# Kernel optimization log

Hardware: AMD Instinct MI355X
Metric: run time of the kernel (lower is better)

## Reference

```python
import jax, jax.numpy as jnp
import numpy as np

NEG_INF = -1.0e12  # matches masked_fill value in the torch module


def _entmax15(x, axis=-1):
    """Exact entmax with alpha=1.5 (Peters & Martins, 2019), sort-based."""
    x = x - jnp.max(x, axis=axis, keepdims=True)
    x = x / 2.0
    d = x.shape[axis]
    xs = -jnp.sort(-x, axis=axis)  # descending sort along normalization axis
    rho = jnp.arange(1, d + 1, dtype=x.dtype)  # 1..d, broadcasts on last axis
    mean = jnp.cumsum(xs, axis=axis) / rho
    mean_sq = jnp.cumsum(xs * xs, axis=axis) / rho
    ss = rho * (mean_sq - mean * mean)
    delta = (1.0 - ss) / rho
    tau = mean - jnp.sqrt(jnp.clip(delta, 0.0))
    support = jnp.sum((tau <= xs).astype(jnp.int32), axis=axis, keepdims=True)
    tau_star = jnp.take_along_axis(tau, support - 1, axis=axis)
    y = jnp.clip(x - tau_star, 0.0)
    return y * y


def setup_inputs() -> dict:
    key = jax.random.key(0)
    kq, kk, kv, km = jax.random.split(key, 4)
    B, H, S, D = 4, 8, 1024, 128
    q = jax.random.normal(kq, (B, H, S, D), dtype=jnp.float32)
    k = jax.random.normal(kk, (B, H, S, D), dtype=jnp.float32)
    v = jax.random.normal(kv, (B, H, S, D), dtype=jnp.float32)
    mask = jax.random.randint(km, (B, 1, S, S), 0, 2, dtype=jnp.int32)
    return {"q": q, "k": k, "v": v, "mask": mask}


def reference(q, k, v, mask):
    D = q.shape[-1]
    scale = 1.0 / jnp.sqrt(jnp.asarray(D, dtype=q.dtype))
    scores = jnp.einsum("bhqd,bhkd->bhqk", q, k) * scale
    scores = jnp.where(mask == 0, jnp.asarray(NEG_INF, dtype=scores.dtype), scores)
    attn = _entmax15(scores, axis=-1)
    return jnp.einsum("bhqk,bhkd->bhqd", attn, v)
```

## Files before the change

### kernel.cpp

```cpp
#include <hip/hip_runtime.h>


#define S_ 1024
#define D_ 128
#define NEG_INF_F (-1.0e12f)
#define SCALE_F 0.08838834764831845f
#define NITER 14
#define CCAP 256

typedef float f32x4 __attribute__((ext_vector_type(4)));
typedef short short8 __attribute__((ext_vector_type(8)));

__device__ __forceinline__ ushort f2bf(float x) {
    unsigned u = __builtin_bit_cast(unsigned, x);
    u += 0x7FFFu + ((u >> 16) & 1u);
    return (ushort)(u >> 16);
}
__device__ __forceinline__ float bf2f(ushort h) {
    unsigned u = ((unsigned)h) << 16;
    return __builtin_bit_cast(float, u);
}

__global__ __launch_bounds__(256)
void pre_cvt(const float* __restrict__ K, const float* __restrict__ V,
             ushort* __restrict__ Kb, ushort* __restrict__ Vt)
{
    __shared__ __align__(16) ushort tileT[64][68];
    const int t = threadIdx.x;
    if (blockIdx.x < 4096) {
        int i = blockIdx.x * 256 + t;
        float4 v = ((const float4*)K)[i];
        ushort4 o;
        o.x = f2bf(v.x); o.y = f2bf(v.y); o.z = f2bf(v.z); o.w = f2bf(v.w);
        ((ushort4*)Kb)[i] = o;
        return;
    }
    const int vb = blockIdx.x - 4096;
    const int bh = vb >> 5, r5 = vb & 31, kt = r5 >> 1, dh = r5 & 1;
    const float* src = V + ((size_t)(bh * S_ + kt * 64)) * D_ + dh * 64;
    #pragma unroll
    for (int i = 0; i < 4; ++i) {
        int idx = t + i * 256, r = idx >> 4, c = idx & 15;
        float4 vv = *(const float4*)(src + (size_t)r * D_ + c * 4);
        tileT[c * 4 + 0][r] = f2bf(vv.x);
        tileT[c * 4 + 1][r] = f2bf(vv.y);
        tileT[c * 4 + 2][r] = f2bf(vv.z);
        tileT[c * 4 + 3][r] = f2bf(vv.w);
    }
    __syncthreads();
    ushort* dst = Vt + ((size_t)(bh * D_ + dh * 64)) * S_ + kt * 64;
    #pragma unroll
    for (int i = 0; i < 2; ++i) {
        int idx = t + i * 256, d = idx >> 3, jj = idx & 7;
        short8 val = *(const short8*)&tileT[d][jj * 8];
        *(short8*)(dst + (size_t)d * S_ + jj * 8) = val;
    }
}

__global__ __launch_bounds__(512, 6)
void entmax_attn(const float* __restrict__ Q, const ushort* __restrict__ Kb,
                 const ushort* __restrict__ Vt, const int* __restrict__ M,
                 float* __restrict__ O)
{
    __shared__ __align__(16) ushort sc[16][1024];
    __shared__ __align__(16) ushort kv[128][64];
    __shared__ __align__(16) ushort q_s[16][128];

    const int t = threadIdx.x;
    const int w = t >> 6, lane = t & 63, l = lane & 15, quad = lane >> 4;
    const int bh = blockIdx.x >> 6, qt = blockIdx.x & 63, b = bh >> 3;

    const ushort* kb_bh = Kb + (size_t)bh * S_ * D_;
    const ushort* vt_bh = Vt + (size_t)bh * D_ * S_;

    const int sr0 = t >> 3, sch = t & 7, sr1 = sr0 + 64;
    ushort* kvw0 = &kv[sr0][(sch ^ (sr0 & 7)) << 3];
    ushort* kvw1 = &kv[sr1][(sch ^ (sr0 & 7)) << 3];

    {
        const float4* qsrc = (const float4*)(Q + ((size_t)bh * S_ + (size_t)qt * 16) * D_);
        int r = t >> 5, c = t & 31;
        float4 v = qsrc[r * 32 + c];
        ushort4 o;
        o.x = f2bf(v.x); o.y = f2bf(v.y); o.z = f2bf(v.z); o.w = f2bf(v.w);
        *(ushort4*)&q_s[r][(((c >> 1) ^ (r & 7)) << 3) + ((c & 1) << 2)] = o;
    }
    short8 s0 = *(const short8*)(kb_bh + (size_t)sr0 * D_ + sch * 8);
    short8 s1 = *(const short8*)(kb_bh + (size_t)sr1 * D_ + sch * 8);
    *(short8*)kvw0 = s0;
    *(short8*)kvw1 = s1;
    __syncthreads();

    short8 aq[4];
    #pragma unroll
    for (int ks = 0; ks < 4; ++ks)
        aq[ks] = *(const short8*)&q_s[l][((ks * 4 + quad) ^ (l & 7)) << 3];

    const int n = w * 16 + l;
    const ushort* kvA = &kv[n][(quad ^ (l & 7)) << 3];
    const ushort* kvB = &kv[n][((4 + quad) ^ (l & 7)) << 3];

    #pragma unroll 1
    for (int kt = 0; kt < 8; ++kt) {
        f32x4 acc = {0.f, 0.f, 0.f, 0.f};
        #pragma unroll
        for (int kh = 0; kh < 2; ++kh) {
            const int h = kt * 2 + kh;
            if (h < 15) {
                const int h2 = h + 1;
                const ushort* nb = kb_bh + (size_t)(h2 >> 1) * (128 * D_) + (h2 & 1) * 64;
                s0 = *(const short8*)(nb + (size_t)sr0 * D_ + sch * 8);
                s1 = *(const short8*)(nb + (size_t)sr1 * D_ + sch * 8);
            }
            __builtin_amdgcn_s_setprio(1);
            {
                short8 bk0 = *(const short8*)kvA;
                short8 bk1 = *(const short8*)kvB;
                acc = __builtin_amdgcn_mfma_f32_16x16x32_bf16(aq[kh * 2 + 0], bk0, acc, 0, 0, 0);
                acc = __builtin_amdgcn_mfma_f32_16x16x32_bf16(aq[kh * 2 + 1], bk1, acc, 0, 0, 0);
            }
            __builtin_amdgcn_s_setprio(0);
            if (kh == 1) {
                #pragma unroll
                for (int r = 0; r < 4; ++r) {
                    const int rr = quad * 4 + r, col = kt * 128 + n;
                    sc[rr][(((col >> 3) ^ (rr & 7)) << 3) + (col & 7)] =
                        f2bf(acc[r] * SCALE_F);
                }
            }
            __syncthreads();
            if (h < 15) {
                *(short8*)kvw0 = s0;
                *(short8*)kvw1 = s1;
                __syncthreads();
            }
        }
    }

    s0 = *(const short8*)(vt_bh + (size_t)sr0 * S_ + sch * 8);
    s1 = *(const short8*)(vt_bh + (size_t)sr1 * S_ + sch * 8);

    const int row = t >> 5, u = t & 31;
    const int qg = qt * 16 + row;
    float x[32];
    #pragma unroll
    for (int c = 0; c < 4; ++c) {
        short8 v8 = *(const short8*)&sc[row][((c * 32 + u) ^ (row & 7)) << 3];
        #pragma unroll
        for (int e = 0; e < 8; ++e) x[c * 8 + e] = bf2f(((ushort*)&v8)[e]);
    }
    {
        const int4* mrow = (const int4*)(M + ((size_t)b * S_ + qg) * S_);
        #pragma unroll
        for (int c = 0; c < 4; ++c) {
            #pragma unroll
            for (int h = 0; h < 2; ++h) {
                int4 mm = mrow[c * 64 + u * 2 + h];
                if (mm.x == 0) x[c * 8 + h * 4 + 0] = NEG_INF_F;
                if (mm.y == 0) x[c * 8 + h * 4 + 1] = NEG_INF_F;
                if (mm.z == 0) x[c * 8 + h * 4 + 2] = NEG_INF_F;
                if (mm.w == 0) x[c * 8 + h * 4 + 3] = NEG_INF_F;
            }
        }
    }
    float mx = -3.0e38f;
    #pragma unroll
    for (int j = 0; j < 32; ++j) mx = fmaxf(mx, x[j]);
    #pragma unroll
    for (int off = 1; off < 32; off <<= 1) mx = fmaxf(mx, __shfl_xor(mx, off));
    #pragma unroll
    for (int j = 0; j < 32; ++j) x[j] = (x[j] - mx) * 0.5f;

    float* cand = (float*)&kv[0][0];
    const unsigned long long halfmask =
        (lane >= 32) ? 0xFFFFFFFF00000000ull : 0x00000000FFFFFFFFull;
    int cnt = 0;
    #pragma unroll
    for (int j = 0; j < 32; ++j) {
        const bool p = (x[j] > -1.0f);
        unsigned long long bal = __ballot(p) & halfmask;
        if (p) {
            int pos = cnt + (int)__builtin_amdgcn_mbcnt_hi(
                (unsigned)(bal >> 32),
                __builtin_amdgcn_mbcnt_lo((unsigned)bal, 0));
            if (pos < CCAP) cand[row * CCAP + pos] = x[j];
        }
        cnt += __popcll(bal);
    }

    float tau;
    if (cnt <= CCAP) {
        const float* crow = cand + row * CCAP;
        float lo = -1.f, hi = 0.f;
        #pragma unroll 1
        for (int it = 0; it < NITER; ++it) {
            const float tm = 0.5f * (lo + hi);
            float f = 0.f;
            for (int j = u; j < cnt; j += 32) {
                float d = fmaxf(crow[j] - tm, 0.f);
                f = fmaf(d, d, f);
            }
            #pragma unroll
            for (int off = 1; off < 32; off <<= 1) f += __shfl_xor(f, off);
            const bool ge = (f >= 1.f);
            lo = ge ? tm : lo;
            hi = ge ? hi : tm;
        }
        tau = 0.5f * (lo + hi);
    } else {
        float lo = -1.f, hi = 0.f;
        #pragma unroll 1
        for (int it = 0; it < NITER; ++it) {
            const float tm = 0.5f * (lo + hi);
            float f = 0.f;
            #pragma unroll
            for (int j = 0; j < 32; ++j) {
                float d = fmaxf(x[j] - tm, 0.f);
                f = fmaf(d, d, f);
            }
            #pragma unroll
            for (int off = 1; off < 32; off <<= 1) f += __shfl_xor(f, off);
            const bool ge = (f >= 1.f);
            lo = ge ? tm : lo;
            hi = ge ? hi : tm;
        }
        tau = 0.5f * (lo + hi);
    }

    #pragma unroll
    for (int c = 0; c < 4; ++c) {
        short8 v8;
        #pragma unroll
        for (int e = 0; e < 8; ++e) {
            float d = fmaxf(x[c * 8 + e] - tau, 0.f);
            ((ushort*)&v8)[e] = f2bf(d * d);
        }
        *(short8*)&sc[row][((c * 32 + u) ^ (row & 7)) << 3] = v8;
    }
    __syncthreads();
    *(short8*)kvw0 = s0;
    *(short8*)kvw1 = s1;
    __syncthreads();

    f32x4 oa = {0.f, 0.f, 0.f, 0.f};
    #pragma unroll 1
    for (int vh = 0; vh < 16; ++vh) {
        if (vh < 15) {
            const ushort* nb = vt_bh + (size_t)(vh + 1) * 64;
            s0 = *(const short8*)(nb + (size_t)sr0 * S_ + sch * 8);
            s1 = *(const short8*)(nb + (size_t)sr1 * S_ + sch * 8);
        }
        __builtin_amdgcn_s_setprio(1);
        {
            short8 ap0 = *(const short8*)&sc[l][((vh * 8 + quad) ^ (l & 7)) << 3];
            short8 ap1 = *(const short8*)&sc[l][((vh * 8 + 4 + quad) ^ (l & 7)) << 3];
            short8 bv0 = *(const short8*)kvA;
            short8 bv1 = *(const short8*)kvB;
            oa = __builtin_amdgcn_mfma_f32_16x16x32_bf16(ap0, bv0, oa, 0, 0, 0);
            oa = __builtin_amdgcn_mfma_f32_16x16x32_bf16(ap1, bv1, oa, 0, 0, 0);
        }
        __builtin_amdgcn_s_setprio(0);
        __syncthreads();
        if (vh < 15) {
            *(short8*)kvw0 = s0;
            *(short8*)kvw1 = s1;
            __syncthreads();
        }
    }

    float* ob = O + ((size_t)bh * S_ + (size_t)qt * 16) * D_;
    #pragma unroll
    for (int r = 0; r < 4; ++r)
        ob[(size_t)(quad * 4 + r) * D_ + w * 16 + l] = oa[r];
}

extern "C" void kernel_launch(void* const* d_in, const int* in_sizes, int n_in,
                              void* d_out, int out_size, void* d_ws, size_t ws_size,
                              hipStream_t stream) {
    const float* q = (const float*)d_in[0];
    const float* k = (const float*)d_in[1];
    const float* v = (const float*)d_in[2];
    const int*   m = (const int*)d_in[3];
    float*       o = (float*)d_out;

    ushort* Kb = (ushort*)d_ws;
    ushort* Vt = (ushort*)((char*)d_ws + 8388608);

    pre_cvt<<<5120, 256, 0, stream>>>(k, v, Kb, Vt);
    entmax_attn<<<2048, 512, 0, stream>>>(q, Kb, Vt, m, o);
}
```

Baseline: 190.4 us.

## Load K/V MFMA operands directly from global into registers, drop LDS staging

Removes the shared-memory staging buffer for K and V tiles. Each wave now loads its MFMA B operands straight from global memory into registers, prefetching one tile ahead, which removes most __syncthreads barriers in the QK and PV loops. The score column mapping is changed so each wave covers a contiguous 16-column slice per 128-key tile. It also drops the candidate-compaction path of the entmax bisection and raises the occupancy hint to 8 blocks. The cost is more redundant global/L2 traffic, since K/V rows are no longer shared through LDS across the block, and more register pressure.

```diff
diff --git a/kernel.cpp b/kernel.cpp
--- a/kernel.cpp
+++ b/kernel.cpp
@@ -6,7 +6,6 @@
 #define NEG_INF_F (-1.0e12f)
 #define SCALE_F 0.08838834764831845f
 #define NITER 14
-#define CCAP 256
 
 typedef float f32x4 __attribute__((ext_vector_type(4)));
 typedef short short8 __attribute__((ext_vector_type(8)));
@@ -57,25 +56,20 @@
     }
 }
 
-__global__ __launch_bounds__(512, 6)
+__global__ __launch_bounds__(512, 8)
 void entmax_attn(const float* __restrict__ Q, const ushort* __restrict__ Kb,
                  const ushort* __restrict__ Vt, const int* __restrict__ M,
                  float* __restrict__ O)
 {
     __shared__ __align__(16) ushort sc[16][1024];
-    __shared__ __align__(16) ushort kv[128][64];
     __shared__ __align__(16) ushort q_s[16][128];
 
     const int t = threadIdx.x;
     const int w = t >> 6, lane = t & 63, l = lane & 15, quad = lane >> 4;
     const int bh = blockIdx.x >> 6, qt = blockIdx.x & 63, b = bh >> 3;
 
-    const ushort* kb_bh = Kb + (size_t)bh * S_ * D_;
-    const ushort* vt_bh = Vt + (size_t)bh * D_ * S_;
-
-    const int sr0 = t >> 3, sch = t & 7, sr1 = sr0 + 64;
-    ushort* kvw0 = &kv[sr0][(sch ^ (sr0 & 7)) << 3];
-    ushort* kvw1 = &kv[sr1][(sch ^ (sr0 & 7)) << 3];
+    const ushort* kb_bh = Kb + (size_t)bh * (S_ * D_);
+    const ushort* vt_bh = Vt + (size_t)bh * (D_ * S_);
 
     {
         const float4* qsrc = (const float4*)(Q + ((size_t)bh * S_ + (size_t)qt * 16) * D_);
@@ -85,10 +79,13 @@
         o.x = f2bf(v.x); o.y = f2bf(v.y); o.z = f2bf(v.z); o.w = f2bf(v.w);
         *(ushort4*)&q_s[r][(((c >> 1) ^ (r & 7)) << 3) + ((c & 1) << 2)] = o;
     }
-    short8 s0 = *(const short8*)(kb_bh + (size_t)sr0 * D_ + sch * 8);
-    short8 s1 = *(const short8*)(kb_bh + (size_t)sr1 * D_ + sch * 8);
-    *(short8*)kvw0 = s0;
-    *(short8*)kvw1 = s1;
+
+    const ushort* kp = kb_bh + (size_t)(w * 16 + l) * D_ + quad * 8;
+    short8 c0 = *(const short8*)(kp +  0);
+    short8 c1 = *(const short8*)(kp + 32);
+    short8 c2 = *(const short8*)(kp + 64);
+    short8 c3 = *(const short8*)(kp + 96);
+
     __syncthreads();
 
     short8 aq[4];
@@ -96,49 +93,44 @@
     for (int ks = 0; ks < 4; ++ks)
         aq[ks] = *(const short8*)&q_s[l][((ks * 4 + quad) ^ (l & 7)) << 3];
 
-    const int n = w * 16 + l;
-    const ushort* kvA = &kv[n][(quad ^ (l & 7)) << 3];
-    const ushort* kvB = &kv[n][((4 + quad) ^ (l & 7)) << 3];
-
     #pragma unroll 1
-    for (int kt = 0; kt < 8; ++kt) {
+    for (int kt = 0; kt < 7; ++kt) {
+        const ushort* np = kp + (size_t)(kt + 1) * (128 * D_);
+        short8 n0 = *(const short8*)(np +  0);
+        short8 n1 = *(const short8*)(np + 32);
+        short8 n2 = *(const short8*)(np + 64);
+        short8 n3 = *(const short8*)(np + 96);
         f32x4 acc = {0.f, 0.f, 0.f, 0.f};
-        #pragma unroll
-        for (int kh = 0; kh < 2; ++kh) {
-            const int h = kt * 2 + kh;
-            if (h < 15) {
-                const int h2 = h + 1;
-                const ushort* nb = kb_bh + (size_t)(h2 >> 1) * (128 * D_) + (h2 & 1) * 64;
-                s0 = *(const short8*)(nb + (size_t)sr0 * D_ + sch * 8);
-                s1 = *(const short8*)(nb + (size_t)sr1 * D_ + sch * 8);
-            }
-            __builtin_amdgcn_s_setprio(1);
-            {
-                short8 bk0 = *(const short8*)kvA;
-                short8 bk1 = *(const short8*)kvB;
-                acc = __builtin_amdgcn_mfma_f32_16x16x32_bf16(aq[kh * 2 + 0], bk0, acc, 0, 0, 0);
-                acc = __builtin_amdgcn_mfma_f32_16x16x32_bf16(aq[kh * 2 + 1], bk1, acc, 0, 0, 0);
-            }
-            __builtin_amdgcn_s_setprio(0);
-            if (kh == 1) {
-                #pragma unroll
-                for (int r = 0; r < 4; ++r) {
-                    const int rr = quad * 4 + r, col = kt * 128 + n;
-                    sc[rr][(((col >> 3) ^ (rr & 7)) << 3) + (col & 7)] =
-                        f2bf(acc[r] * SCALE_F);
-                }
-            }
-            __syncthreads();
-            if (h < 15) {
-                *(short8*)kvw0 = s0;
-                *(short8*)kvw1 = s1;
-                __syncthreads();
-            }
-        }
-    }
-
-    s0 = *(const short8*)(vt_bh + (size_t)sr0 * S_ + sch * 8);
-    s1 = *(const short8*)(vt_bh + (size_t)sr1 * S_ + sch * 8);
+        __builtin_amdgcn_s_setprio(1);
+        acc = __builtin_amdgcn_mfma_f32_16x16x32_bf16(aq[0], c0, acc, 0, 0, 0);
+        acc = __builtin_amdgcn_mfma_f32_16x16x32_bf16(aq[1], c1, acc, 0, 0, 0);
+        acc = __builtin_amdgcn_mfma_f32_16x16x32_bf16(aq[2], c2, acc, 0, 0, 0);
+        acc = __builtin_amdgcn_mfma_f32_16x16x32_bf16(aq[3], c3, acc, 0, 0, 0);
+        __builtin_amdgcn_s_setprio(0);
+        const int coln = kt * 16 + w * 2 + (l >> 3);
+        #pragma unroll
+        for (int r = 0; r < 4; ++r) {
+            const int rr = quad * 4 + r;
+            sc[rr][((coln ^ (rr & 7)) << 3) + (l & 7)] = f2bf(acc[r] * SCALE_F);
+        }
+        c0 = n0; c1 = n1; c2 = n2; c3 = n3;
+    }
+    {
+        f32x4 acc = {0.f, 0.f, 0.f, 0.f};
+        __builtin_amdgcn_s_setprio(1);
+        acc = __builtin_amdgcn_mfma_f32_16x16x32_bf16(aq[0], c0, acc, 0, 0, 0);
+        acc = __builtin_amdgcn_mfma_f32_16x16x32_bf16(aq[1], c1, acc, 0, 0, 0);
+        acc = __builtin_amdgcn_mfma_f32_16x16x32_bf16(aq[2], c2, acc, 0, 0, 0);
+        acc = __builtin_amdgcn_mfma_f32_16x16x32_bf16(aq[3], c3, acc, 0, 0, 0);
+        __builtin_amdgcn_s_setprio(0);
+        const int coln = 7 * 16 + w * 2 + (l >> 3);
+        #pragma unroll
+        for (int r = 0; r < 4; ++r) {
+            const int rr = quad * 4 + r;
+            sc[rr][((coln ^ (rr & 7)) << 3) + (l & 7)] = f2bf(acc[r] * SCALE_F);
+        }
+    }
+    __syncthreads();
 
     const int row = t >> 5, u = t & 31;
     const int qg = qt * 16 + row;
@@ -171,61 +163,23 @@
     #pragma unroll
     for (int j = 0; j < 32; ++j) x[j] = (x[j] - mx) * 0.5f;
 
-    float* cand = (float*)&kv[0][0];
-    const unsigned long long halfmask =
-        (lane >= 32) ? 0xFFFFFFFF00000000ull : 0x00000000FFFFFFFFull;
-    int cnt = 0;
-    #pragma unroll
-    for (int j = 0; j < 32; ++j) {
-        const bool p = (x[j] > -1.0f);
-        unsigned long long bal = __ballot(p) & halfmask;
-        if (p) {
-            int pos = cnt + (int)__builtin_amdgcn_mbcnt_hi(
-                (unsigned)(bal >> 32),
-                __builtin_amdgcn_mbcnt_lo((unsigned)bal, 0));
-            if (pos < CCAP) cand[row * CCAP + pos] = x[j];
-        }
-        cnt += __popcll(bal);
-    }
-
-    float tau;
-    if (cnt <= CCAP) {
-        const float* crow = cand + row * CCAP;
-        float lo = -1.f, hi = 0.f;
-        #pragma unroll 1
-        for (int it = 0; it < NITER; ++it) {
-            const float tm = 0.5f * (lo + hi);
-            float f = 0.f;
-            for (int j = u; j < cnt; j += 32) {
-                float d = fmaxf(crow[j] - tm, 0.f);
-                f = fmaf(d, d, f);
-            }
-            #pragma unroll
-            for (int off = 1; off < 32; off <<= 1) f += __shfl_xor(f, off);
-            const bool ge = (f >= 1.f);
-            lo = ge ? tm : lo;
-            hi = ge ? hi : tm;
-        }
-        tau = 0.5f * (lo + hi);
-    } else {
-        float lo = -1.f, hi = 0.f;
-        #pragma unroll 1
-        for (int it = 0; it < NITER; ++it) {
-            const float tm = 0.5f * (lo + hi);
-            float f = 0.f;
-            #pragma unroll
-            for (int j = 0; j < 32; ++j) {
-                float d = fmaxf(x[j] - tm, 0.f);
-                f = fmaf(d, d, f);
-            }
-            #pragma unroll
-            for (int off = 1; off < 32; off <<= 1) f += __shfl_xor(f, off);
-            const bool ge = (f >= 1.f);
-            lo = ge ? tm : lo;
-            hi = ge ? hi : tm;
-        }
-        tau = 0.5f * (lo + hi);
-    }
+    float lo = -1.f, hi = 0.f;
+    #pragma unroll 1
+    for (int it = 0; it < NITER; ++it) {
+        const float tm = 0.5f * (lo + hi);
+        float f = 0.f;
+        #pragma unroll
+        for (int j = 0; j < 32; ++j) {
+            float d = fmaxf(x[j] - tm, 0.f);
+            f = fmaf(d, d, f);
+        }
+        #pragma unroll
+        for (int off = 1; off < 32; off <<= 1) f += __shfl_xor(f, off);
+        const bool ge = (f >= 1.f);
+        lo = ge ? tm : lo;
+        hi = ge ? hi : tm;
+    }
+    const float tau = 0.5f * (lo + hi);
 
     #pragma unroll
     for (int c = 0; c < 4; ++c) {
@@ -237,35 +191,45 @@
         }
         *(short8*)&sc[row][((c * 32 + u) ^ (row & 7)) << 3] = v8;
     }
-    __syncthreads();
-    *(short8*)kvw0 = s0;
-    *(short8*)kvw1 = s1;
+
+    const ushort* vp = vt_bh + (size_t)(w * 16 + l) * S_ + quad * 8;
+    c0 = *(const short8*)(vp +  0);
+    c1 = *(const short8*)(vp + 32);
+    c2 = *(const short8*)(vp + 64);
+    c3 = *(const short8*)(vp + 96);
     __syncthreads();
 
     f32x4 oa = {0.f, 0.f, 0.f, 0.f};
     #pragma unroll 1
-    for (int vh = 0; vh < 16; ++vh) {
-        if (vh < 15) {
-            const ushort* nb = vt_bh + (size_t)(vh + 1) * 64;
-            s0 = *(const short8*)(nb + (size_t)sr0 * S_ + sch * 8);
-            s1 = *(const short8*)(nb + (size_t)sr1 * S_ + sch * 8);
-        }
-        __builtin_amdgcn_s_setprio(1);
-        {
-            short8 ap0 = *(const short8*)&sc[l][((vh * 8 + quad) ^ (l & 7)) << 3];
-            short8 ap1 = *(const short8*)&sc[l][((vh * 8 + 4 + quad) ^ (l & 7)) << 3];
-            short8 bv0 = *(const short8*)kvA;
-            short8 bv1 = *(const short8*)kvB;
-            oa = __builtin_amdgcn_mfma_f32_16x16x32_bf16(ap0, bv0, oa, 0, 0, 0);
-            oa = __builtin_amdgcn_mfma_f32_16x16x32_bf16(ap1, bv1, oa, 0, 0, 0);
-        }
-        __builtin_amdgcn_s_setprio(0);
-        __syncthreads();
-        if (vh < 15) {
-            *(short8*)kvw0 = s0;
-            *(short8*)kvw1 = s1;
-            __syncthreads();
-        }
+    for (int vt = 0; vt < 7; ++vt) {
+        const ushort* np = vp + (size_t)(vt + 1) * 128;
+        short8 n0 = *(const short8*)(np +  0);
+        short8 n1 = *(const short8*)(np + 32);
+        short8 n2 = *(const short8*)(np + 64);
+        short8 n3 = *(const short8*)(np + 96);
+        short8 a0 = *(const short8*)&sc[l][((vt * 16 +  0 + quad) ^ (l & 7)) << 3];
+        short8 a1 = *(const short8*)&sc[l][((vt * 16 +  4 + quad) ^ (l & 7)) << 3];
+        short8 a2 = *(const short8*)&sc[l][((vt * 16 +  8 + quad) ^ (l & 7)) << 3];
+        short8 a3 = *(const short8*)&sc[l][((vt * 16 + 12 + quad) ^ (l & 7)) << 3];
+        __builtin_amdgcn_s_setprio(1);
+        oa = __builtin_amdgcn_mfma_f32_16x16x32_bf16(a0, c0, oa, 0, 0, 0);
+        oa = __builtin_amdgcn_mfma_f32_16x16x32_bf16(a1, c1, oa, 0, 0, 0);
+        oa = __builtin_amdgcn_mfma_f32_16x16x32_bf16(a2, c2, oa, 0, 0, 0);
+        oa = __builtin_amdgcn_mfma_f32_16x16x32_bf16(a3, c3, oa, 0, 0, 0);
+        __builtin_amdgcn_s_setprio(0);
+        c0 = n0; c1 = n1; c2 = n2; c3 = n3;
+    }
+    {
+        short8 a0 = *(const short8*)&sc[l][((7 * 16 +  0 + quad) ^ (l & 7)) << 3];
+        short8 a1 = *(const short8*)&sc[l][((7 * 16 +  4 + quad) ^ (l & 7)) << 3];
+        short8 a2 = *(const short8*)&sc[l][((7 * 16 +  8 + quad) ^ (l & 7)) << 3];
+        short8 a3 = *(const short8*)&sc[l][((7 * 16 + 12 + quad) ^ (l & 7)) << 3];
+        __builtin_amdgcn_s_setprio(1);
+        oa = __builtin_amdgcn_mfma_f32_16x16x32_bf16(a0, c0, oa, 0, 0, 0);
+        oa = __builtin_amdgcn_mfma_f32_16x16x32_bf16(a1, c1, oa, 0, 0, 0);
+        oa = __builtin_amdgcn_mfma_f32_16x16x32_bf16(a2, c2, oa, 0, 0, 0);
+        oa = __builtin_amdgcn_mfma_f32_16x16x32_bf16(a3, c3, oa, 0, 0, 0);
+        __builtin_amdgcn_s_setprio(0);
     }
 
     float* ob = O + ((size_t)bh * S_ + (size_t)qt * 16) * D_;
```

Measured after the change: 226.9 us. +19.2%, slower.

## Pre-swizzle K/V tiles and stream them via async global-to-LDS triple buffering

Applied to the files above, without the earlier changes.

The pre-conversion kernel now writes K and transposed V into per-warp, XOR-swizzled 64-column tiles, so each wave can copy its own slice straight into LDS with global_load_lds. A three-deep LDS ring with vmcnt waits replaces the register staging and the two __syncthreads per step, for both the QK and PV loops. Q is converted directly into MFMA fragments in registers instead of going through LDS, and the entmax candidate buffer reuses the score row with a larger cap. LDS use grows (occupancy bound drops to 2) and correctness now depends on each wave reading only the data it loaded itself, and on the hand-written waitcnt counts.

```diff
diff --git a/kernel.cpp b/kernel.cpp
--- a/kernel.cpp
+++ b/kernel.cpp
@@ -6,7 +6,7 @@
 #define NEG_INF_F (-1.0e12f)
 #define SCALE_F 0.08838834764831845f
 #define NITER 14
-#define CCAP 256
+#define CCAP 512
 
 typedef float f32x4 __attribute__((ext_vector_type(4)));
 typedef short short8 __attribute__((ext_vector_type(8)));
@@ -19,6 +19,17 @@
 __device__ __forceinline__ float bf2f(ushort h) {
     unsigned u = ((unsigned)h) << 16;
     return __builtin_bit_cast(float, u);
+}
+__device__ __forceinline__ short8 cvt8(float4 a, float4 b) {
+    short8 r; ushort* p = (ushort*)&r;
+    p[0] = f2bf(a.x); p[1] = f2bf(a.y); p[2] = f2bf(a.z); p[3] = f2bf(a.w);
+    p[4] = f2bf(b.x); p[5] = f2bf(b.y); p[6] = f2bf(b.z); p[7] = f2bf(b.w);
+    return r;
+}
+__device__ __forceinline__ void gload16(const ushort* g, ushort* l) {
+    __builtin_amdgcn_global_load_lds(
+        (const __attribute__((address_space(1))) void*)g,
+        (__attribute__((address_space(3))) void*)l, 16, 0, 0);
 }
 
 __global__ __launch_bounds__(256)
@@ -27,15 +38,21 @@
 {
     __shared__ __align__(16) ushort tileT[64][68];
     const int t = threadIdx.x;
-    if (blockIdx.x < 4096) {
-        int i = blockIdx.x * 256 + t;
-        float4 v = ((const float4*)K)[i];
-        ushort4 o;
-        o.x = f2bf(v.x); o.y = f2bf(v.y); o.z = f2bf(v.z); o.w = f2bf(v.w);
-        ((ushort4*)Kb)[i] = o;
+    if (blockIdx.x < 2048) {
+        const int u   = blockIdx.x * 256 + t;
+        const int c   = u & 15;
+        const int key = (u >> 4) & 1023;
+        const int bh  = u >> 14;
+        const int row = key & 127, kt = key >> 7;
+        const int h   = kt * 2 + (c >> 3), c_lo = c & 7;
+        const float* s = K + ((size_t)(bh * S_ + key)) * D_ + c * 8;
+        float4 a = *(const float4*)s, b2 = *(const float4*)(s + 4);
+        short8 o = cvt8(a, b2);
+        *(short8*)(Kb + (((size_t)(bh * 16 + h) * 128 + row) * 8 +
+                         (c_lo ^ (row & 7))) * 8) = o;
         return;
     }
-    const int vb = blockIdx.x - 4096;
+    const int vb = blockIdx.x - 2048;
     const int bh = vb >> 5, r5 = vb & 31, kt = r5 >> 1, dh = r5 & 1;
     const float* src = V + ((size_t)(bh * S_ + kt * 64)) * D_ + dh * 64;
     #pragma unroll
@@ -48,97 +65,85 @@
         tileT[c * 4 + 3][r] = f2bf(vv.w);
     }
     __syncthreads();
-    ushort* dst = Vt + ((size_t)(bh * D_ + dh * 64)) * S_ + kt * 64;
     #pragma unroll
     for (int i = 0; i < 2; ++i) {
         int idx = t + i * 256, d = idx >> 3, jj = idx & 7;
         short8 val = *(const short8*)&tileT[d][jj * 8];
-        *(short8*)(dst + (size_t)d * S_ + jj * 8) = val;
-    }
-}
-
-__global__ __launch_bounds__(512, 6)
+        *(short8*)(Vt + (((size_t)(bh * 16 + kt) * 128 + dh * 64 + d) * 8 +
+                         (jj ^ (d & 7))) * 8) = val;
+    }
+}
+
+__global__ __launch_bounds__(512, 2)
 void entmax_attn(const float* __restrict__ Q, const ushort* __restrict__ Kb,
                  const ushort* __restrict__ Vt, const int* __restrict__ M,
                  float* __restrict__ O)
 {
     __shared__ __align__(16) ushort sc[16][1024];
-    __shared__ __align__(16) ushort kv[128][64];
-    __shared__ __align__(16) ushort q_s[16][128];
+    __shared__ __align__(16) ushort kv[3][128][64];
 
     const int t = threadIdx.x;
     const int w = t >> 6, lane = t & 63, l = lane & 15, quad = lane >> 4;
     const int bh = blockIdx.x >> 6, qt = blockIdx.x & 63, b = bh >> 3;
 
-    const ushort* kb_bh = Kb + (size_t)bh * S_ * D_;
-    const ushort* vt_bh = Vt + (size_t)bh * D_ * S_;
-
-    const int sr0 = t >> 3, sch = t & 7, sr1 = sr0 + 64;
-    ushort* kvw0 = &kv[sr0][(sch ^ (sr0 & 7)) << 3];
-    ushort* kvw1 = &kv[sr1][(sch ^ (sr0 & 7)) << 3];
-
+    const ushort* kb_h = Kb + (size_t)bh * (16 * 128 * 64);
+    const ushort* vt_h = Vt + (size_t)bh * (16 * 128 * 64);
+
+    const int n = w * 16 + l;
+    const int chA = ((quad) ^ (l & 7)) * 8;
+    const int chB = ((4 + quad) ^ (l & 7)) * 8;
+
+    auto stg = [&](int s, int buf) {
+        const ushort* g = (s < 16 ? kb_h + (size_t)s * 8192
+                                  : vt_h + (size_t)(s - 16) * 8192)
+                          + w * 1024 + lane * 8;
+        ushort* ld = &kv[buf][w * 16][0];
+        gload16(g, ld);
+        gload16(g + 512, ld + 512);
+    };
+
+    stg(0, 0); stg(1, 1); stg(2, 2);
+    short8 aq[4];
     {
-        const float4* qsrc = (const float4*)(Q + ((size_t)bh * S_ + (size_t)qt * 16) * D_);
-        int r = t >> 5, c = t & 31;
-        float4 v = qsrc[r * 32 + c];
-        ushort4 o;
-        o.x = f2bf(v.x); o.y = f2bf(v.y); o.z = f2bf(v.z); o.w = f2bf(v.w);
-        *(ushort4*)&q_s[r][(((c >> 1) ^ (r & 7)) << 3) + ((c & 1) << 2)] = o;
-    }
-    short8 s0 = *(const short8*)(kb_bh + (size_t)sr0 * D_ + sch * 8);
-    short8 s1 = *(const short8*)(kb_bh + (size_t)sr1 * D_ + sch * 8);
-    *(short8*)kvw0 = s0;
-    *(short8*)kvw1 = s1;
-    __syncthreads();
-
-    short8 aq[4];
-    #pragma unroll
-    for (int ks = 0; ks < 4; ++ks)
-        aq[ks] = *(const short8*)&q_s[l][((ks * 4 + quad) ^ (l & 7)) << 3];
-
-    const int n = w * 16 + l;
-    const ushort* kvA = &kv[n][(quad ^ (l & 7)) << 3];
-    const ushort* kvB = &kv[n][((4 + quad) ^ (l & 7)) << 3];
-
-    #pragma unroll 1
-    for (int kt = 0; kt < 8; ++kt) {
-        f32x4 acc = {0.f, 0.f, 0.f, 0.f};
+        const float* qr = Q + ((size_t)(bh * S_ + qt * 16 + l)) * D_ + quad * 8;
         #pragma unroll
-        for (int kh = 0; kh < 2; ++kh) {
-            const int h = kt * 2 + kh;
-            if (h < 15) {
-                const int h2 = h + 1;
-                const ushort* nb = kb_bh + (size_t)(h2 >> 1) * (128 * D_) + (h2 & 1) * 64;
-                s0 = *(const short8*)(nb + (size_t)sr0 * D_ + sch * 8);
-                s1 = *(const short8*)(nb + (size_t)sr1 * D_ + sch * 8);
-            }
+        for (int ks = 0; ks < 4; ++ks) {
+            float4 qa = *(const float4*)(qr + ks * 32);
+            float4 qb = *(const float4*)(qr + ks * 32 + 4);
+            aq[ks] = cvt8(qa, qb);
+        }
+    }
+
+    f32x4 acc = {0.f, 0.f, 0.f, 0.f};
+    {
+        int bufc = 0;
+        #pragma unroll 1
+        for (int s = 0; s < 16; ++s) {
+            asm volatile("s_waitcnt vmcnt(4)" ::: "memory");
+            short8 bk0 = *(const short8*)&kv[bufc][n][chA];
+            short8 bk1 = *(const short8*)&kv[bufc][n][chB];
+            const int dh = s & 1;
+            if (dh == 0) { acc[0] = acc[1] = acc[2] = acc[3] = 0.f; }
             __builtin_amdgcn_s_setprio(1);
-            {
-                short8 bk0 = *(const short8*)kvA;
-                short8 bk1 = *(const short8*)kvB;
-                acc = __builtin_amdgcn_mfma_f32_16x16x32_bf16(aq[kh * 2 + 0], bk0, acc, 0, 0, 0);
-                acc = __builtin_amdgcn_mfma_f32_16x16x32_bf16(aq[kh * 2 + 1], bk1, acc, 0, 0, 0);
-            }
+            acc = __builtin_amdgcn_mfma_f32_16x16x32_bf16(aq[dh * 2 + 0], bk0, acc, 0, 0, 0);
+            acc = __builtin_amdgcn_mfma_f32_16x16x32_bf16(aq[dh * 2 + 1], bk1, acc, 0, 0, 0);
             __builtin_amdgcn_s_setprio(0);
-            if (kh == 1) {
+            if (dh == 1) {
+                const int coln = (s >> 1) * 16 + w * 2 + (l >> 3);
                 #pragma unroll
                 for (int r = 0; r < 4; ++r) {
-                    const int rr = quad * 4 + r, col = kt * 128 + n;
-                    sc[rr][(((col >> 3) ^ (rr & 7)) << 3) + (col & 7)] =
+                    const int rr = quad * 4 + r;
+                    sc[rr][((coln ^ (rr & 7)) << 3) + (l & 7)] =
                         f2bf(acc[r] * SCALE_F);
                 }
             }
-            __syncthreads();
-            if (h < 15) {
-                *(short8*)kvw0 = s0;
-                *(short8*)kvw1 = s1;
-                __syncthreads();
-            }
-        }
-    }
-
-    s0 = *(const short8*)(vt_bh + (size_t)sr0 * S_ + sch * 8);
-    s1 = *(const short8*)(vt_bh + (size_t)sr1 * S_ + sch * 8);
+            asm volatile("" ::: "memory");
+            stg(s + 3, bufc);
+            bufc = (bufc == 2) ? 0 : bufc + 1;
+        }
+    }
+    asm volatile("s_waitcnt lgkmcnt(0)" ::: "memory");
+    __builtin_amdgcn_s_barrier();
 
     const int row = t >> 5, u = t & 31;
     const int qg = qt * 16 + row;
@@ -171,7 +176,7 @@
     #pragma unroll
     for (int j = 0; j < 32; ++j) x[j] = (x[j] - mx) * 0.5f;
 
-    float* cand = (float*)&kv[0][0];
+    float* cand = (float*)&sc[row][0];
     const unsigned long long halfmask =
         (lane >= 32) ? 0xFFFFFFFF00000000ull : 0x00000000FFFFFFFFull;
     int cnt = 0;
@@ -183,21 +188,20 @@
             int pos = cnt + (int)__builtin_amdgcn_mbcnt_hi(
                 (unsigned)(bal >> 32),
                 __builtin_amdgcn_mbcnt_lo((unsigned)bal, 0));
-            if (pos < CCAP) cand[row * CCAP + pos] = x[j];
+            if (pos < CCAP) cand[pos] = x[j];
         }
         cnt += __popcll(bal);
     }
 
     float tau;
     if (cnt <= CCAP) {
-        const float* crow = cand + row * CCAP;
         float lo = -1.f, hi = 0.f;
         #pragma unroll 1
         for (int it = 0; it < NITER; ++it) {
             const float tm = 0.5f * (lo + hi);
             float f = 0.f;
             for (int j = u; j < cnt; j += 32) {
-                float d = fmaxf(crow[j] - tm, 0.f);
+                float d = fmaxf(cand[j] - tm, 0.f);
                 f = fmaf(d, d, f);
             }
             #pragma unroll
@@ -237,34 +241,45 @@
         }
         *(short8*)&sc[row][((c * 32 + u) ^ (row & 7)) << 3] = v8;
     }
-    __syncthreads();
-    *(short8*)kvw0 = s0;
-    *(short8*)kvw1 = s1;
-    __syncthreads();
+    asm volatile("s_waitcnt lgkmcnt(0)" ::: "memory");
+    __builtin_amdgcn_s_barrier();
 
     f32x4 oa = {0.f, 0.f, 0.f, 0.f};
-    #pragma unroll 1
-    for (int vh = 0; vh < 16; ++vh) {
-        if (vh < 15) {
-            const ushort* nb = vt_bh + (size_t)(vh + 1) * 64;
-            s0 = *(const short8*)(nb + (size_t)sr0 * S_ + sch * 8);
-            s1 = *(const short8*)(nb + (size_t)sr1 * S_ + sch * 8);
-        }
-        __builtin_amdgcn_s_setprio(1);
-        {
+    {
+        int bufc = 1;
+        #pragma unroll 1
+        for (int s = 16; s < 30; ++s) {
+            asm volatile("s_waitcnt vmcnt(4)" ::: "memory");
+            const int vh = s - 16;
+            short8 bv0 = *(const short8*)&kv[bufc][n][chA];
+            short8 bv1 = *(const short8*)&kv[bufc][n][chB];
             short8 ap0 = *(const short8*)&sc[l][((vh * 8 + quad) ^ (l & 7)) << 3];
             short8 ap1 = *(const short8*)&sc[l][((vh * 8 + 4 + quad) ^ (l & 7)) << 3];
-            short8 bv0 = *(const short8*)kvA;
-            short8 bv1 = *(const short8*)kvB;
+            __builtin_amdgcn_s_setprio(1);
             oa = __builtin_amdgcn_mfma_f32_16x16x32_bf16(ap0, bv0, oa, 0, 0, 0);
             oa = __builtin_amdgcn_mfma_f32_16x16x32_bf16(ap1, bv1, oa, 0, 0, 0);
-        }
-        __builtin_amdgcn_s_setprio(0);
-        __syncthreads();
-        if (vh < 15) {
-            *(short8*)kvw0 = s0;
-            *(short8*)kvw1 = s1;
-            __syncthreads();
+            __builtin_amdgcn_s_setprio(0);
+            asm volatile("" ::: "memory");
+            if (s < 29) stg(s + 3, bufc);
+            bufc = (bufc == 2) ? 0 : bufc + 1;
+        }
+        {
+            asm volatile("s_waitcnt vmcnt(2)" ::: "memory");
+            short8 bv0 = *(const short8*)&kv[0][n][chA];
+            short8 bv1 = *(const short8*)&kv[0][n][chB];
+            short8 ap0 = *(const short8*)&sc[l][((14 * 8 + quad) ^ (l & 7)) << 3];
+            short8 ap1 = *(const short8*)&sc[l][((14 * 8 + 4 + quad) ^ (l & 7)) << 3];
+            oa = __builtin_amdgcn_mfma_f32_16x16x32_bf16(ap0, bv0, oa, 0, 0, 0);
+            oa = __builtin_amdgcn_mfma_f32_16x16x32_bf16(ap1, bv1, oa, 0, 0, 0);
+        }
+        {
+            asm volatile("s_waitcnt vmcnt(0)" ::: "memory");
+            short8 bv0 = *(const short8*)&kv[1][n][chA];
+            short8 bv1 = *(const short8*)&kv[1][n][chB];
+            short8 ap0 = *(const short8*)&sc[l][((15 * 8 + quad) ^ (l & 7)) << 3];
+            short8 ap1 = *(const short8*)&sc[l][((15 * 8 + 4 + quad) ^ (l & 7)) << 3];
+            oa = __builtin_amdgcn_mfma_f32_16x16x32_bf16(ap0, bv0, oa, 0, 0, 0);
+            oa = __builtin_amdgcn_mfma_f32_16x16x32_bf16(ap1, bv1, oa, 0, 0, 0);
         }
     }
 
@@ -286,6 +301,6 @@
     ushort* Kb = (ushort*)d_ws;
     ushort* Vt = (ushort*)((char*)d_ws + 8388608);
 
-    pre_cvt<<<5120, 256, 0, stream>>>(k, v, Kb, Vt);
+    pre_cvt<<<3072, 256, 0, stream>>>(k, v, Kb, Vt);
     entmax_attn<<<2048, 512, 0, stream>>>(q, Kb, Vt, m, o);
 }
```

Result: slower. 606.8 us (+218.7%).
